# Optimization experiments

Measured on AMD Instinct MI355X. Metric: run time of the kernel, lower is better.

Reference implementation:

```python
import jax, jax.numpy as jnp
import numpy as np

GAMMA_NEG = 4.0
GAMMA_POS = 0.0
B, C = 128, 1024


def setup_inputs() -> dict:
    key = jax.random.key(0)
    k1, k2, k3 = jax.random.split(key, 3)
    # probabilities strictly inside (0,1) so log(x) and log(1-x) are finite
    x = jax.random.uniform(k1, (B, C), jnp.float32, 0.05, 0.95)
    # sparse multi-label binary targets (float, as in torch)
    y = (jax.random.uniform(k2, (B, C)) < 0.05).astype(jnp.float32)
    # binary coherence mask with self-coherence on the diagonal
    mask = (jax.random.uniform(k3, (C, C)) < 0.1).astype(jnp.float32)
    mask = jnp.maximum(mask, jnp.eye(C, dtype=jnp.float32))
    return {"x": x, "y": y, "mask": mask}


def reference(x, y, mask):
    # prepare_input:
    #   masked[b,i,j] = mask[i,j] * x[b,j]
    #   out_y[b,1,j]  = x[b,j] * y[b,j]
    #   max_masked_outy[b,i] = max_j mask[i,j] * x[b,j]^2 * y[b,j]
    prod = (x * x * y)[:, None, :] * mask[None, :, :]   # [B, C, C]
    mm = jnp.max(prod, axis=2)                           # [B, C]
    xp = (1.0 - y) * x + y * mm                          # [B, C]
    # ASL focal loss
    loss_pos = y * jnp.power(1.0 - xp, GAMMA_POS) * jnp.log(xp)
    loss_neg = (1.0 - y) * jnp.power(xp, GAMMA_NEG) * jnp.log(1.0 - xp)
    return -jnp.mean(loss_pos + loss_neg)
```

## Files before the change

kernel.cpp:

```cpp
#include <hip/hip_runtime.h>
#include <math.h>

#define BB 128
#define CC 1024
#define SPLIT 32
#define NBLK (BB * SPLIT)
#define INV_N (1.0f / (float)(BB * CC))

__global__ __launch_bounds__(64) void asl_main_kernel(
    const float* __restrict__ x, const float* __restrict__ y,
    const float* __restrict__ mask, float* __restrict__ partial) {
  const int blk   = blockIdx.x;
  const int b     = blk & (BB - 1);
  const int chunk = blk >> 7;
  const int lane  = threadIdx.x;

  __shared__ unsigned short jidx[CC];
  __shared__ float          jw[CC];

  const float* xb = x + (size_t)b * CC;
  const float* yb = y + (size_t)b * CC;

  const float4* x4 = (const float4*)xb;
  const float4* y4 = (const float4*)yb;
  float4 xq[4], yq[4];
#pragma unroll
  for (int c = 0; c < 4; ++c) {
    xq[c] = x4[lane + 64 * c];
    yq[c] = y4[lane + 64 * c];
  }

  int base = 0;
#pragma unroll
  for (int c = 0; c < 4; ++c) {
    const float yv[4] = {yq[c].x, yq[c].y, yq[c].z, yq[c].w};
    const float xv[4] = {xq[c].x, xq[c].y, xq[c].z, xq[c].w};
#pragma unroll
    for (int q = 0; q < 4; ++q) {
      const bool p = (yv[q] != 0.0f);
      const unsigned long long bal = __ballot(p);
      if (p) {
        const int pos = base + __popcll(bal & ((1ull << lane) - 1ull));
        jidx[pos] = (unsigned short)(4 * (lane + 64 * c) + q);
        jw[pos]   = xv[q] * xv[q];
      }
      base += __popcll(bal);
    }
  }
  const int n = base;

  float acc = 0.0f;

  for (int e = chunk; e < n; e += SPLIT) {
    const int ii = jidx[e];
    const float* mrow = mask + (size_t)ii * CC;
    float mm = 0.0f;
    for (int k = lane; k < n; k += 64)
      mm = fmaxf(mm, mrow[jidx[k]] * jw[k]);
#pragma unroll
    for (int o = 32; o > 0; o >>= 1)
      mm = fmaxf(mm, __shfl_xor(mm, o, 64));
    if (lane == 0) acc += logf(mm);
  }

  if (chunk < 16) {
    const int   i  = chunk * 64 + lane;
    const float xi = xb[i];
    const float yi = yb[i];
    if (yi == 0.0f) {
      const float x2 = xi * xi;
      acc += (x2 * x2) * logf(1.0f - xi);
    }
  }

#pragma unroll
  for (int o = 32; o > 0; o >>= 1)
    acc += __shfl_down(acc, o, 64);
  if (lane == 0) partial[blk] = acc;
}

__global__ __launch_bounds__(256) void asl_final_kernel(
    const float* __restrict__ partial, float* __restrict__ out) {
  const int tid = threadIdx.x;
  const float4* p4 = (const float4*)partial;
  float v = 0.0f;
#pragma unroll
  for (int r = 0; r < NBLK / 4 / 256; ++r) {
    const float4 q = p4[tid + 256 * r];
    v += (q.x + q.y) + (q.z + q.w);
  }
#pragma unroll
  for (int o = 32; o > 0; o >>= 1)
    v += __shfl_down(v, o, 64);
  __shared__ float s[4];
  if ((tid & 63) == 0) s[tid >> 6] = v;
  __syncthreads();
  if (tid == 0) out[0] = -(s[0] + s[1] + s[2] + s[3]) * INV_N;
}

extern "C" void kernel_launch(void* const* d_in, const int* in_sizes, int n_in,
                              void* d_out, int out_size, void* d_ws, size_t ws_size,
                              hipStream_t stream) {
  const float* x    = (const float*)d_in[0];
  const float* y    = (const float*)d_in[1];
  const float* mask = (const float*)d_in[2];
  float* out     = (float*)d_out;
  float* partial = (float*)d_ws;

  asl_main_kernel<<<NBLK, 64, 0, stream>>>(x, y, mask, partial);
  asl_final_kernel<<<1, 256, 0, stream>>>(partial, out);
}
```

Baseline: 12.28 us.

## Double split, compact positives via per-lane bitmask scan, exit idle blocks early

Doubles the per-row block split, so each block handles fewer positive labels. Positive compaction now gives each lane 16 contiguous elements and uses a bitmask plus a wave prefix scan instead of 16 ballots. Blocks with no positive work and no negative-term slice exit right after loading y, before x is read. The weight buffer is capped at 256 entries, with a fallback that reloads x from global memory, which cuts LDS use but adds a branch and doubles the number of launched blocks.

```diff
diff --git a/kernel.cpp b/kernel.cpp
--- a/kernel.cpp
+++ b/kernel.cpp
@@ -3,8 +3,9 @@
 
 #define BB 128
 #define CC 1024
-#define SPLIT 32
+#define SPLIT 64
 #define NBLK (BB * SPLIT)
+#define CAP 256
 #define INV_N (1.0f / (float)(BB * CC))
 
 __global__ __launch_bounds__(64) void asl_main_kernel(
@@ -16,38 +17,55 @@
   const int lane  = threadIdx.x;
 
   __shared__ unsigned short jidx[CC];
-  __shared__ float          jw[CC];
+  __shared__ float          jw[CAP];
 
   const float* xb = x + (size_t)b * CC;
   const float* yb = y + (size_t)b * CC;
 
-  const float4* x4 = (const float4*)xb;
   const float4* y4 = (const float4*)yb;
-  float4 xq[4], yq[4];
+  float4 yq[4];
 #pragma unroll
-  for (int c = 0; c < 4; ++c) {
-    xq[c] = x4[lane + 64 * c];
-    yq[c] = y4[lane + 64 * c];
+  for (int c = 0; c < 4; ++c) yq[c] = y4[4 * lane + c];
+  const float yv[16] = {yq[0].x, yq[0].y, yq[0].z, yq[0].w,
+                        yq[1].x, yq[1].y, yq[1].z, yq[1].w,
+                        yq[2].x, yq[2].y, yq[2].z, yq[2].w,
+                        yq[3].x, yq[3].y, yq[3].z, yq[3].w};
+  unsigned m = 0;
+#pragma unroll
+  for (int t = 0; t < 16; ++t) m |= (yv[t] != 0.0f) ? (1u << t) : 0u;
+  const int cnt = __popc(m);
+
+  int inc = cnt;
+#pragma unroll
+  for (int o = 1; o < 64; o <<= 1) {
+    const int t = __shfl_up(inc, o, 64);
+    if (lane >= o) inc += t;
+  }
+  const int n     = __shfl(inc, 63, 64);
+  const int base0 = inc - cnt;
+
+  if (chunk >= 16 && chunk >= n) {
+    if (lane == 0) partial[blk] = 0.0f;
+    return;
   }
 
-  int base = 0;
+  const float4* x4 = (const float4*)xb;
+  float4 xq[4];
 #pragma unroll
-  for (int c = 0; c < 4; ++c) {
-    const float yv[4] = {yq[c].x, yq[c].y, yq[c].z, yq[c].w};
-    const float xv[4] = {xq[c].x, xq[c].y, xq[c].z, xq[c].w};
+  for (int c = 0; c < 4; ++c) xq[c] = x4[4 * lane + c];
+  const float xv[16] = {xq[0].x, xq[0].y, xq[0].z, xq[0].w,
+                        xq[1].x, xq[1].y, xq[1].z, xq[1].w,
+                        xq[2].x, xq[2].y, xq[2].z, xq[2].w,
+                        xq[3].x, xq[3].y, xq[3].z, xq[3].w};
+  int pos = base0;
 #pragma unroll
-    for (int q = 0; q < 4; ++q) {
-      const bool p = (yv[q] != 0.0f);
-      const unsigned long long bal = __ballot(p);
-      if (p) {
-        const int pos = base + __popcll(bal & ((1ull << lane) - 1ull));
-        jidx[pos] = (unsigned short)(4 * (lane + 64 * c) + q);
-        jw[pos]   = xv[q] * xv[q];
-      }
-      base += __popcll(bal);
+  for (int t = 0; t < 16; ++t) {
+    if (m & (1u << t)) {
+      jidx[pos] = (unsigned short)(16 * lane + t);
+      if (pos < CAP) jw[pos] = xv[t] * xv[t];
+      ++pos;
     }
   }
-  const int n = base;
 
   float acc = 0.0f;
 
@@ -55,8 +73,13 @@
     const int ii = jidx[e];
     const float* mrow = mask + (size_t)ii * CC;
     float mm = 0.0f;
-    for (int k = lane; k < n; k += 64)
-      mm = fmaxf(mm, mrow[jidx[k]] * jw[k]);
+    for (int k = lane; k < n; k += 64) {
+      const int j = jidx[k];
+      float w;
+      if (k < CAP) w = jw[k];
+      else { const float xg = xb[j]; w = xg * xg; }
+      mm = fmaxf(mm, mrow[j] * w);
+    }
 #pragma unroll
     for (int o = 32; o > 0; o >>= 1)
       mm = fmaxf(mm, __shfl_xor(mm, o, 64));
```

Result: slower. 14.05 us (+14.3%).

## Replace sparse gather with dense coalesced mask row scans, four rows at a time

Applied to the files above, without the earlier changes.

Removes the shared-memory compaction of positive labels and the indirect gather of mask entries. Each block now owns a 64-column window of one batch row, builds a bitmask of positive labels with ballots, and for each positive reads the full mask row with coalesced float4 loads. It processes four rows per iteration and merges their max reductions with paired half-wave shuffles. The split per batch row drops from 32 to 16 blocks. This trades more mask bytes read (dense rows instead of only the positive columns) for coalesced access, memory-level parallelism and no LDS traffic.

```diff
diff --git a/kernel.cpp b/kernel.cpp
--- a/kernel.cpp
+++ b/kernel.cpp
@@ -3,73 +3,126 @@
 
 #define BB 128
 #define CC 1024
-#define SPLIT 32
+#define SPLIT 16
 #define NBLK (BB * SPLIT)
 #define INV_N (1.0f / (float)(BB * CC))
+
+__device__ __forceinline__ unsigned long long spread4(unsigned long long u) {
+  u &= 0xFFFFull;
+  u = (u | (u << 24)) & 0x000000FF000000FFull;
+  u = (u | (u << 12)) & 0x000F000F000F000Full;
+  u = (u | (u << 6))  & 0x0303030303030303ull;
+  u = (u | (u << 3))  & 0x1111111111111111ull;
+  return u;
+}
 
 __global__ __launch_bounds__(64) void asl_main_kernel(
     const float* __restrict__ x, const float* __restrict__ y,
     const float* __restrict__ mask, float* __restrict__ partial) {
-  const int blk   = blockIdx.x;
-  const int b     = blk & (BB - 1);
-  const int chunk = blk >> 7;
-  const int lane  = threadIdx.x;
+  const int blk  = blockIdx.x;
+  const int b    = blk >> 4;
+  const int c    = blk & 15;
+  const int lane = threadIdx.x;
 
-  __shared__ unsigned short jidx[CC];
-  __shared__ float          jw[CC];
+  const float4* x4 = (const float4*)(x + (size_t)b * CC);
+  const float4* y4 = (const float4*)(y + (size_t)b * CC);
 
-  const float* xb = x + (size_t)b * CC;
-  const float* yb = y + (size_t)b * CC;
-
-  const float4* x4 = (const float4*)xb;
-  const float4* y4 = (const float4*)yb;
   float4 xq[4], yq[4];
 #pragma unroll
-  for (int c = 0; c < 4; ++c) {
-    xq[c] = x4[lane + 64 * c];
-    yq[c] = y4[lane + 64 * c];
+  for (int cc = 0; cc < 4; ++cc) {
+    xq[cc] = x4[lane + 64 * cc];
+    yq[cc] = y4[lane + 64 * cc];
   }
 
-  int base = 0;
+  float w[4][4];
 #pragma unroll
-  for (int c = 0; c < 4; ++c) {
-    const float yv[4] = {yq[c].x, yq[c].y, yq[c].z, yq[c].w};
-    const float xv[4] = {xq[c].x, xq[c].y, xq[c].z, xq[c].w};
-#pragma unroll
-    for (int q = 0; q < 4; ++q) {
-      const bool p = (yv[q] != 0.0f);
-      const unsigned long long bal = __ballot(p);
-      if (p) {
-        const int pos = base + __popcll(bal & ((1ull << lane) - 1ull));
-        jidx[pos] = (unsigned short)(4 * (lane + 64 * c) + q);
-        jw[pos]   = xv[q] * xv[q];
-      }
-      base += __popcll(bal);
-    }
+  for (int cc = 0; cc < 4; ++cc) {
+    w[cc][0] = xq[cc].x * xq[cc].x * yq[cc].x;
+    w[cc][1] = xq[cc].y * xq[cc].y * yq[cc].y;
+    w[cc][2] = xq[cc].z * xq[cc].z * yq[cc].z;
+    w[cc][3] = xq[cc].w * xq[cc].w * yq[cc].w;
   }
-  const int n = base;
+
+  const int cc0 = c >> 2;
+  const int l0  = 16 * (c & 3);
+  float4 wx, wy;
+  switch (cc0) {
+    case 0: wx = xq[0]; wy = yq[0]; break;
+    case 1: wx = xq[1]; wy = yq[1]; break;
+    case 2: wx = xq[2]; wy = yq[2]; break;
+    default: wx = xq[3]; wy = yq[3]; break;
+  }
+  const bool win = (lane >= l0) && (lane < l0 + 16);
+
+  const unsigned long long b0 = __ballot(win && (wy.x != 0.0f));
+  const unsigned long long b1 = __ballot(win && (wy.y != 0.0f));
+  const unsigned long long b2 = __ballot(win && (wy.z != 0.0f));
+  const unsigned long long b3 = __ballot(win && (wy.w != 0.0f));
+  unsigned long long M =  spread4(b0 >> l0)        | (spread4(b1 >> l0) << 1) |
+                         (spread4(b2 >> l0) << 2)  | (spread4(b3 >> l0) << 3);
 
   float acc = 0.0f;
 
-  for (int e = chunk; e < n; e += SPLIT) {
-    const int ii = jidx[e];
-    const float* mrow = mask + (size_t)ii * CC;
-    float mm = 0.0f;
-    for (int k = lane; k < n; k += 64)
-      mm = fmaxf(mm, mrow[jidx[k]] * jw[k]);
-#pragma unroll
-    for (int o = 32; o > 0; o >>= 1)
-      mm = fmaxf(mm, __shfl_xor(mm, o, 64));
-    if (lane == 0) acc += logf(mm);
+  if (win) {
+    if (wy.x == 0.0f) { const float t = wx.x * wx.x; acc += t * t * logf(1.0f - wx.x); }
+    if (wy.y == 0.0f) { const float t = wx.y * wx.y; acc += t * t * logf(1.0f - wx.y); }
+    if (wy.z == 0.0f) { const float t = wx.z * wx.z; acc += t * t * logf(1.0f - wx.z); }
+    if (wy.w == 0.0f) { const float t = wx.w * wx.w; acc += t * t * logf(1.0f - wx.w); }
   }
 
-  if (chunk < 16) {
-    const int   i  = chunk * 64 + lane;
-    const float xi = xb[i];
-    const float yi = yb[i];
-    if (yi == 0.0f) {
-      const float x2 = xi * xi;
-      acc += (x2 * x2) * logf(1.0f - xi);
+  while (M) {
+    int t0 = __builtin_ctzll(M); M &= M - 1;
+    int live = 1, t1 = t0, t2 = t0, t3 = t0;
+    if (M) { t1 = __builtin_ctzll(M); M &= M - 1; live = 2;
+      if (M) { t2 = __builtin_ctzll(M); M &= M - 1; live = 3;
+        if (M) { t3 = __builtin_ctzll(M); M &= M - 1; live = 4; } } }
+
+    const float4* r0 = (const float4*)(mask + (size_t)(64 * c + t0) * CC);
+    const float4* r1 = (const float4*)(mask + (size_t)(64 * c + t1) * CC);
+    const float4* r2 = (const float4*)(mask + (size_t)(64 * c + t2) * CC);
+    const float4* r3 = (const float4*)(mask + (size_t)(64 * c + t3) * CC);
+
+    float4 v0[4], v1[4], v2[4], v3[4];
+#pragma unroll
+    for (int cc = 0; cc < 4; ++cc) {
+      v0[cc] = r0[lane + 64 * cc];
+      v1[cc] = r1[lane + 64 * cc];
+      v2[cc] = r2[lane + 64 * cc];
+      v3[cc] = r3[lane + 64 * cc];
+    }
+    float mm0 = 0.0f, mm1 = 0.0f, mm2 = 0.0f, mm3 = 0.0f;
+#pragma unroll
+    for (int cc = 0; cc < 4; ++cc) {
+      mm0 = fmaxf(mm0, fmaxf(fmaxf(v0[cc].x * w[cc][0], v0[cc].y * w[cc][1]),
+                             fmaxf(v0[cc].z * w[cc][2], v0[cc].w * w[cc][3])));
+      mm1 = fmaxf(mm1, fmaxf(fmaxf(v1[cc].x * w[cc][0], v1[cc].y * w[cc][1]),
+                             fmaxf(v1[cc].z * w[cc][2], v1[cc].w * w[cc][3])));
+      mm2 = fmaxf(mm2, fmaxf(fmaxf(v2[cc].x * w[cc][0], v2[cc].y * w[cc][1]),
+                             fmaxf(v2[cc].z * w[cc][2], v2[cc].w * w[cc][3])));
+      mm3 = fmaxf(mm3, fmaxf(fmaxf(v3[cc].x * w[cc][0], v3[cc].y * w[cc][1]),
+                             fmaxf(v3[cc].z * w[cc][2], v3[cc].w * w[cc][3])));
+    }
+
+    float u = (lane < 32) ? mm0 : mm1;
+    float v = (lane < 32) ? mm1 : mm0;
+    v = __shfl_xor(v, 32, 64);
+    u = fmaxf(u, v);
+#pragma unroll
+    for (int o = 16; o > 0; o >>= 1)
+      u = fmaxf(u, __shfl_xor(u, o, 64));
+    if (lane == 0)               acc += logf(u);
+    if (lane == 32 && live >= 2) acc += logf(u);
+
+    if (live >= 3) {
+      float p = (lane < 32) ? mm2 : mm3;
+      float q = (lane < 32) ? mm3 : mm2;
+      q = __shfl_xor(q, 32, 64);
+      p = fmaxf(p, q);
+#pragma unroll
+      for (int o = 16; o > 0; o >>= 1)
+        p = fmaxf(p, __shfl_xor(p, o, 64));
+      if (lane == 1)               acc += logf(p);
+      if (lane == 33 && live >= 4) acc += logf(p);
     }
   }
 
```

Result: slower. 13.70 us (+11.5%).

## Process four mask rows per wavefront iteration and halve block split

Applied to the files above, without the earlier changes.

Halves the number of blocks per batch row (SPLIT 32→16) so every block now also handles a 64-element slice of the negative-loss term. Each wavefront now gathers four positive-label mask rows per loop iteration, sharing the jidx/jw loads and overlapping gather latency. The cross-lane max reductions are paired so two rows reduce together with one extra xor-32 shuffle. The x/y loads for the negative term are hoisted ahead of the compaction. Fewer blocks means less parallelism and more per-block work, and with about 51 positives per row the 4-way batching can leave a tail iteration only partly filled.

```diff
diff --git a/kernel.cpp b/kernel.cpp
--- a/kernel.cpp
+++ b/kernel.cpp
@@ -3,7 +3,7 @@
 
 #define BB 128
 #define CC 1024
-#define SPLIT 32
+#define SPLIT 16
 #define NBLK (BB * SPLIT)
 #define INV_N (1.0f / (float)(BB * CC))
 
@@ -30,6 +30,10 @@
     yq[c] = y4[lane + 64 * c];
   }
 
+  const int   i  = chunk * 64 + lane;
+  const float xi = xb[i];
+  const float yi = yb[i];
+
   int base = 0;
 #pragma unroll
   for (int c = 0; c < 4; ++c) {
@@ -51,26 +55,50 @@
 
   float acc = 0.0f;
 
-  for (int e = chunk; e < n; e += SPLIT) {
-    const int ii = jidx[e];
-    const float* mrow = mask + (size_t)ii * CC;
-    float mm = 0.0f;
-    for (int k = lane; k < n; k += 64)
-      mm = fmaxf(mm, mrow[jidx[k]] * jw[k]);
+  for (int e = chunk; e < n; e += 4 * SPLIT) {
+    const int  e1 = e + SPLIT,  e2 = e + 2 * SPLIT,  e3 = e + 3 * SPLIT;
+    const bool h1 = (e1 < n),   h2 = (e2 < n),       h3 = (e3 < n);
+    const float* r0 = mask + (size_t)jidx[e] * CC;
+    const float* r1 = h1 ? mask + (size_t)jidx[e1] * CC : r0;
+    const float* r2 = h2 ? mask + (size_t)jidx[e2] * CC : r0;
+    const float* r3 = h3 ? mask + (size_t)jidx[e3] * CC : r0;
+
+    float mm0 = 0.0f, mm1 = 0.0f, mm2 = 0.0f, mm3 = 0.0f;
+    for (int k = lane; k < n; k += 64) {
+      const int   j = jidx[k];
+      const float w = jw[k];
+      mm0 = fmaxf(mm0, r0[j] * w);
+      mm1 = fmaxf(mm1, r1[j] * w);
+      mm2 = fmaxf(mm2, r2[j] * w);
+      mm3 = fmaxf(mm3, r3[j] * w);
+    }
+
+    float u = (lane < 32) ? mm0 : mm1;
+    float v = (lane < 32) ? mm1 : mm0;
+    v = __shfl_xor(v, 32, 64);
+    u = fmaxf(u, v);
 #pragma unroll
-    for (int o = 32; o > 0; o >>= 1)
-      mm = fmaxf(mm, __shfl_xor(mm, o, 64));
-    if (lane == 0) acc += logf(mm);
+    for (int o = 16; o > 0; o >>= 1)
+      u = fmaxf(u, __shfl_xor(u, o, 64));
+    if (lane == 0)        acc += logf(u);
+    if (lane == 32 && h1) acc += logf(u);
+
+    if (h2) {
+      float p = (lane < 32) ? mm2 : mm3;
+      float q = (lane < 32) ? mm3 : mm2;
+      q = __shfl_xor(q, 32, 64);
+      p = fmaxf(p, q);
+#pragma unroll
+      for (int o = 16; o > 0; o >>= 1)
+        p = fmaxf(p, __shfl_xor(p, o, 64));
+      if (lane == 1)        acc += logf(p);
+      if (lane == 33 && h3) acc += logf(p);
+    }
   }
 
-  if (chunk < 16) {
-    const int   i  = chunk * 64 + lane;
-    const float xi = xb[i];
-    const float yi = yb[i];
-    if (yi == 0.0f) {
-      const float x2 = xi * xi;
-      acc += (x2 * x2) * logf(1.0f - xi);
-    }
+  if (yi == 0.0f) {
+    const float x2 = xi * xi;
+    acc += (x2 * x2) * logf(1.0f - xi);
   }
 
 #pragma unroll
```

Measured after the change: 11.44 us. 6.8% less time.
